# Performance work log

Hardware: AMD Instinct MI355X
Metric: run time of the kernel (lower is better)

## Reference

```python
import jax, jax.numpy as jnp
import numpy as np

BETA = 0.2
ALPHA_NEG = 0.8
ALPHA_POS = 0.2
EPS = 1e-8  # torch cosine_similarity eps

B, D, P = 8192, 256, 4096


def setup_inputs() -> dict:
    key = jax.random.key(0)
    k1, k2 = jax.random.split(key)
    embeddings = jax.random.normal(k1, (B, D), dtype=jnp.float32)
    positive_pairs = jax.random.randint(k2, (P, 2), 0, B, dtype=jnp.int32)
    return {"embeddings": embeddings, "positive_pairs": positive_pairs}


def reference(embeddings, positive_pairs):
    b = embeddings.shape[0]
    p = positive_pairs.shape[0]
    # cosine similarity matrix (normalize once, single GEMM)
    nrm = jnp.maximum(jnp.linalg.norm(embeddings, axis=1, keepdims=True), EPS)
    e = embeddings / nrm
    cos = e @ e.T                              # [B, B]
    exp_cos = jnp.exp(cos / BETA)
    ii = positive_pairs[:, 0]
    jj = positive_pairs[:, 1]
    # mask = eye + positive pairs (both directions)
    mask = jnp.eye(b, dtype=bool)
    mask = mask.at[ii, jj].set(True).at[jj, ii].set(True)
    exp_masked = jnp.where(mask, 0.0, exp_cos)  # masked_fill(mask, 0)
    pos_ij = exp_cos[ii, jj]                   # [P]
    pos_ji = exp_cos[jj, ii]                   # [P]
    exp_i = exp_masked[ii]                     # [P, B]
    exp_j = exp_masked[jj]                     # [P, B]
    # hard-negative mining via alpha_neg quantile per row
    thr_i = jnp.quantile(exp_i, ALPHA_NEG, axis=1, keepdims=True)
    thr_j = jnp.quantile(exp_j, ALPHA_NEG, axis=1, keepdims=True)
    S_i = jnp.sum(jnp.where(exp_i >= thr_i, exp_i, 0.0), axis=1)  # [P]
    S_j = jnp.sum(jnp.where(exp_j >= thr_j, exp_j, 0.0), axis=1)  # [P]
    # hard-positive mining via alpha_pos quantile
    thr_pij = jnp.quantile(pos_ij, ALPHA_POS)
    thr_pji = jnp.quantile(pos_ji, ALPHA_POS)
    sel_ij = pos_ij <= thr_pij
    sel_ji = pos_ji <= thr_pji
    # torch loop zips the two (order-preserving) boolean-selected lists ->
    # truncates to min count; values are never cross-coupled, only the count.
    kmin = jnp.minimum(sel_ij.sum(), sel_ji.sum())
    act_ij = sel_ij & ((jnp.cumsum(sel_ij.astype(jnp.int32)) - 1) < kmin)
    act_ji = sel_ji & ((jnp.cumsum(sel_ji.astype(jnp.int32)) - 1) < kmin)
    # -log(pk / (pk + S[m])) = log1p(S[m] / pk), summed over all m per pk
    term_ij = jnp.log1p(S_i[None, :] / pos_ij[:, None])  # [P, P]
    term_ji = jnp.log1p(S_j[None, :] / pos_ji[:, None])  # [P, P]
    loss = (jnp.sum(term_ij * act_ij[:, None].astype(term_ij.dtype))
            + jnp.sum(term_ji * act_ji[:, None].astype(term_ji.dtype)))
    return loss / (2.0 * p)
```

## Files before the change

### kernel.cpp

```cpp
#include <hip/hip_runtime.h>
#include <stdint.h>

#define BN    8192
#define DK    256
#define PN    4096
#define MAXP  16
#define RANK_ASC 6553
#define QSTEP 0.02f
#define QINV  50.0f

typedef __bf16  bf16_8 __attribute__((ext_vector_type(8)));
typedef __bf16  bf16_4 __attribute__((ext_vector_type(4)));
typedef float   f32x4  __attribute__((ext_vector_type(4)));

__device__ __forceinline__ void gload_lds16(const void* g, void* l) {
  __builtin_amdgcn_global_load_lds(
      (const __attribute__((address_space(1))) unsigned int*)g,
      (__attribute__((address_space(3))) unsigned int*)l, 16, 0, 0);
}

__global__ void prep_clear_kernel(int* pcount, int* rowlist, int* cnt) {
  const int i = blockIdx.x * 256 + threadIdx.x;
  if (i < BN) { pcount[i] = 0; rowlist[i] = 0; }
  if (i == 0) cnt[0] = 0;
}

__global__ void prep_pairs_kernel(const int2* __restrict__ pairs,
                                  int* pcount, int* partners) {
  const int p = blockIdx.x * 256 + threadIdx.x;
  if (p >= PN) return;
  int2 pr = pairs[p];
  int ix = atomicAdd(&pcount[pr.x], 1);
  if (ix < MAXP) partners[pr.x * MAXP + ix] = pr.y;
  int iy = atomicAdd(&pcount[pr.y], 1);
  if (iy < MAXP) partners[pr.y * MAXP + iy] = pr.x;
}

__global__ void prep_compact_kernel(const int* __restrict__ pcount,
                                    int* rowlist, int* cnt) {
  const int i = blockIdx.x * 256 + threadIdx.x;
  if (i < BN && pcount[i] > 0) {
    int pos = atomicAdd(cnt, 1);
    rowlist[pos] = i;
  }
}

__global__ void __launch_bounds__(256) normalize_kernel(
    const float* __restrict__ X, float* __restrict__ E, __bf16* __restrict__ Ebf) {
  const int tid  = threadIdx.x;
  const int lane = tid & 63;
  const int w    = tid >> 6;
  const int row  = blockIdx.x * 4 + w;
  float4 x = ((const float4*)(X + (size_t)row * DK))[lane];
  float ss = x.x * x.x + x.y * x.y + x.z * x.z + x.w * x.w;
  #pragma unroll
  for (int o = 32; o; o >>= 1) ss += __shfl_xor(ss, o);
  float nrm = fmaxf(sqrtf(ss), 1e-8f);
  float4 e;
  e.x = x.x / nrm; e.y = x.y / nrm; e.z = x.z / nrm; e.w = x.w / nrm;
  ((float4*)(E + (size_t)row * DK))[lane] = e;
  bf16_4 b;
  b[0] = (__bf16)e.x; b[1] = (__bf16)e.y; b[2] = (__bf16)e.z; b[3] = (__bf16)e.w;
  *(bf16_4*)(Ebf + (size_t)row * DK + lane * 4) = b;
}

__global__ void __launch_bounds__(256) pos_kernel(
    const float* __restrict__ E, const int2* __restrict__ pairs, float* __restrict__ pos) {
  const int tid  = threadIdx.x;
  const int lane = tid & 63;
  const int w    = tid >> 6;
  const int p    = blockIdx.x * 4 + w;
  int2 pr = pairs[p];
  float4 a = ((const float4*)(E + (size_t)pr.x * DK))[lane];
  float4 b = ((const float4*)(E + (size_t)pr.y * DK))[lane];
  float d = a.x * b.x + a.y * b.y + a.z * b.z + a.w * b.w;
  #pragma unroll
  for (int o = 32; o; o >>= 1) d += __shfl_xor(d, o);
  if (lane == 0) pos[p] = __expf(5.0f * d);
}

__device__ __forceinline__ void find_bin_256(const unsigned* hist, int rank,
                                             int* sh, unsigned* wtot) {
  const int tid = threadIdx.x, lane = tid & 63, w = tid >> 6;
  unsigned x = hist[tid];
  unsigned pref = x;
  #pragma unroll
  for (int o = 1; o < 64; o <<= 1) {
    unsigned y = __shfl_up(pref, o);
    if (lane >= o) pref += y;
  }
  if (lane == 63) wtot[w] = pref;
  __syncthreads();
  unsigned woff = 0;
  for (int i = 0; i < w; ++i) woff += wtot[i];
  unsigned incl = pref + woff, excl = incl - x;
  if ((unsigned)rank >= excl && (unsigned)rank < incl) { sh[0] = tid; sh[1] = rank - (int)excl; }
  __syncthreads();
}

__global__ void __launch_bounds__(256) gemm_code_kernel(
    const __bf16* __restrict__ E, const int* __restrict__ rowlist,
    const int* __restrict__ countp, uint32_t* __restrict__ out4) {
  if ((int)blockIdx.y * 128 >= *countp) return;
  __shared__ __align__(16) __bf16 sA[128 * 32];
  __shared__ __align__(16) __bf16 sB[128 * 32];
  const int tid  = threadIdx.x;
  const int lane = tid & 63;
  const int w    = tid >> 6;
  const int wm   = w >> 1, wn = w & 1;
  const int trow = blockIdx.y * 128;
  const int tcol = blockIdx.x * 128;
  const int r0   = tid >> 2;
  const int seg  = tid & 3;

  const int ga0 = rowlist[trow + r0];
  const int ga1 = rowlist[trow + 64 + r0];
  const __bf16* pa0 = E + (size_t)ga0 * DK + seg * 8;
  const __bf16* pa1 = E + (size_t)ga1 * DK + seg * 8;
  const __bf16* pb0 = E + (size_t)(tcol + r0) * DK + seg * 8;
  const __bf16* pb1 = E + (size_t)(tcol + 64 + r0) * DK + seg * 8;
  __bf16* la0 = &sA[tid * 8];
  __bf16* la1 = &sA[2048 + tid * 8];
  __bf16* lb0 = &sB[tid * 8];
  __bf16* lb1 = &sB[2048 + tid * 8];

  f32x4 acc[4][4];
  #pragma unroll
  for (int i = 0; i < 4; ++i)
    #pragma unroll
    for (int j = 0; j < 4; ++j) {
      f32x4 z = {0.f, 0.f, 0.f, 0.f};
      acc[i][j] = z;
    }

  for (int kt = 0; kt < 8; ++kt) {
    const int k0 = kt * 32;
    __syncthreads();
    gload_lds16(pa0 + k0, la0);
    gload_lds16(pa1 + k0, la1);
    gload_lds16(pb0 + k0, lb0);
    gload_lds16(pb1 + k0, lb1);
    __syncthreads();
    bf16_8 af[4], bfg[4];
    #pragma unroll
    for (int t = 0; t < 4; ++t) {
      af[t]  = *(const bf16_8*)&sA[(wm * 64 + t * 16 + (lane & 15)) * 32 + (lane >> 4) * 8];
      bfg[t] = *(const bf16_8*)&sB[(wn * 64 + t * 16 + (lane & 15)) * 32 + (lane >> 4) * 8];
    }
    #pragma unroll
    for (int i = 0; i < 4; ++i)
      #pragma unroll
      for (int j = 0; j < 4; ++j)
        acc[i][j] = __builtin_amdgcn_mfma_f32_16x16x32_bf16(af[i], bfg[j], acc[i][j], 0, 0, 0);
  }

  const int crow = trow + wm * 64 + (lane >> 4) * 4;
  const int ccol = tcol + wn * 64 + (lane & 15);
  #pragma unroll
  for (int i = 0; i < 4; ++i) {
    const int gidx = (crow + i * 16) >> 2;
    #pragma unroll
    for (int j = 0; j < 4; ++j) {
      const int col = ccol + j * 16;
      uint32_t u = 0;
      #pragma unroll
      for (int r = 0; r < 4; ++r) {
        int c = (int)rintf(fmaf(acc[i][j][r], 250.0f, 128.0f));
        c = c < 1 ? 1 : (c > 255 ? 255 : c);
        u |= (uint32_t)c << (8 * r);
      }
      out4[(size_t)gidx * BN + col] = u;
    }
  }
}

__global__ void __launch_bounds__(256) row_stats4_kernel(
    const uint32_t* __restrict__ expc4, const int* __restrict__ rowlist,
    const int* __restrict__ countp, const int* __restrict__ pcount,
    const int* __restrict__ partners, float* __restrict__ S) {
  __shared__ unsigned hist[4][4][256];
  __shared__ unsigned total[4][256];
  __shared__ int plist[4][MAXP + 1];
  __shared__ int npl[4];
  __shared__ int growl[4];
  __shared__ int sh[2];
  __shared__ unsigned wtot[4];
  __shared__ float redf[4];
  const int g = blockIdx.x;
  const int cnt = *countp;
  if (g * 4 >= cnt) return;
  const int tid = threadIdx.x, lane = tid & 63, w = tid >> 6;

  uint4 rv[8];
  const uint4* src = (const uint4*)(expc4 + (size_t)g * BN);
  #pragma unroll
  for (int q = 0; q < 8; ++q) rv[q] = src[q * 256 + tid];

  if (tid < 4) {
    int rr = g * 4 + tid;
    int grow = (rr < cnt) ? rowlist[rr] : -1;
    growl[tid] = grow;
    int np = 0;
    if (grow >= 0) {
      np = pcount[grow]; if (np > MAXP) np = MAXP;
      for (int e = 0; e < np; ++e) plist[tid][e] = partners[grow * MAXP + e];
      plist[tid][np] = grow;
      np++;
    }
    npl[tid] = np;
  }
  #pragma unroll
  for (int k = 0; k < 16; ++k) ((unsigned*)hist)[k * 256 + tid] = 0;
  __syncthreads();

  #pragma unroll
  for (int r4 = 0; r4 < 4; ++r4) {
    const int np = npl[r4];
    for (int e = 0; e < np; ++e) {
      int c = plist[r4][e];
      int t = c >> 2;
      if ((t & 255) == tid) {
        unsigned* wp = (unsigned*)&rv[t >> 8];
        wp[c & 3] &= ~(0xFFu << (r4 * 8));
      }
    }
  }

  unsigned* h = (unsigned*)hist[w];
  #pragma unroll
  for (int q = 0; q < 8; ++q) {
    #pragma unroll
    for (int word = 0; word < 4; ++word) {
      unsigned dw = ((const unsigned*)&rv[q])[word];
      atomicAdd(&h[0 * 256 + (dw & 255u)], 1u);
      atomicAdd(&h[1 * 256 + ((dw >> 8) & 255u)], 1u);
      atomicAdd(&h[2 * 256 + ((dw >> 16) & 255u)], 1u);
      atomicAdd(&h[3 * 256 + (dw >> 24)], 1u);
    }
  }
  __syncthreads();
  #pragma unroll
  for (int r4 = 0; r4 < 4; ++r4)
    total[r4][tid] = hist[0][r4][tid] + hist[1][r4][tid] + hist[2][r4][tid] + hist[3][r4][tid];
  __syncthreads();

  const float val = __expf((float)(tid - 128) * QSTEP);

  for (int r4 = 0; r4 < 4; ++r4) {
    find_bin_256(total[r4], RANK_ASC, sh, wtot);
    const int b    = sh[0];
    const int need = (int)total[r4][b] - sh[1];
    float contrib = (tid > b) ? (float)total[r4][tid] * val
                  : (tid == b) ? (float)need * val : 0.f;
    #pragma unroll
    for (int o = 32; o; o >>= 1) contrib += __shfl_xor(contrib, o);
    __syncthreads();
    if (lane == 0) redf[w] = contrib;
    __syncthreads();
    if (tid == 0 && growl[r4] >= 0)
      S[growl[r4]] = redf[0] + redf[1] + redf[2] + redf[3];
    __syncthreads();
  }
}

__device__ __forceinline__ float block_sum4(float x, float* red4) {
  const int lane = threadIdx.x & 63, w = threadIdx.x >> 6;
  #pragma unroll
  for (int o = 32; o; o >>= 1) x += __shfl_xor(x, o);
  __syncthreads();
  if (lane == 0) red4[w] = x;
  __syncthreads();
  return red4[0] + red4[1] + red4[2] + red4[3];
}

__global__ void __launch_bounds__(256) finale_kernel(
    const float* __restrict__ pos, const int2* __restrict__ pairs,
    const float* __restrict__ S, float* __restrict__ out) {
  __shared__ uint32_t v[PN];
  __shared__ unsigned hist[256];
  __shared__ int sh[2];
  __shared__ unsigned wtot[4];
  __shared__ float red4[4];
  const int tid = threadIdx.x;
  for (int i = tid; i < PN; i += 256) v[i] = ((const uint32_t*)pos)[i];
  __syncthreads();

  int rank = 819;
  uint32_t prefix = 0;
  for (int pass = 0; pass < 4; ++pass) {
    const int shift = 24 - pass * 8;
    hist[tid] = 0;
    __syncthreads();
    for (int i = tid; i < PN; i += 256) {
      uint32_t x = v[i];
      bool match = (pass == 0) || ((x >> (shift + 8)) == (prefix >> (shift + 8)));
      if (match) atomicAdd(&hist[(x >> shift) & 255u], 1u);
    }
    __syncthreads();
    find_bin_256(hist, rank, sh, wtot);
    prefix |= ((uint32_t)sh[0]) << shift;
    rank = sh[1];
    __syncthreads();
  }
  float thr; __builtin_memcpy(&thr, &prefix, 4);

  float n = 0.f, sl = 0.f, sp = 0.f, sp2 = 0.f;
  for (int r = tid; r < PN; r += 256) {
    float p; uint32_t b = v[r]; __builtin_memcpy(&p, &b, 4);
    if (p <= thr) { n += 1.f; sl += __logf(p); sp += p; sp2 += p * p; }
  }
  float t = 0.f, u = 0.f, vv = 0.f;
  for (int c = tid; c < PN; c += 256) {
    int2 pr = pairs[c];
    float s1 = S[pr.x], s2 = S[pr.y];
    float i1 = 1.f / s1, i2 = 1.f / s2;
    t += __logf(s1) + __logf(s2);
    u += i1 + i2;
    vv += i1 * i1 + i2 * i2;
  }
  const float N  = block_sum4(n, red4);
  const float SL = block_sum4(sl, red4);
  const float SP = block_sum4(sp, red4);
  const float SP2= block_sum4(sp2, red4);
  const float T  = block_sum4(t, red4);
  const float U  = block_sum4(u, red4);
  const float V  = block_sum4(vv, red4);
  if (tid == 0) {
    double num = (double)N * T - 2.0 * (double)PN * (double)SL
               + (double)SP * U - 0.5 * (double)SP2 * V;
    out[0] = (float)(num / (2.0 * (double)PN));
  }
}

extern "C" void kernel_launch(void* const* d_in, const int* in_sizes, int n_in,
                              void* d_out, int out_size, void* d_ws, size_t ws_size,
                              hipStream_t stream) {
  const float* emb  = (const float*)d_in[0];
  const int2* pairs = (const int2*)d_in[1];
  float* out = (float*)d_out;

  char* w = (char*)d_ws;
  size_t off = 0;
  float*    E     = (float*)(w + off);    off += (size_t)BN * DK * 4;
  __bf16*   Ebf   = (__bf16*)(w + off);   off += (size_t)BN * DK * 2;
  float*    S     = (float*)(w + off);    off += (size_t)BN * 4;
  float*    pos   = (float*)(w + off);    off += (size_t)PN * 4;
  int*      pcnt  = (int*)(w + off);      off += (size_t)BN * 4;
  int*      parts = (int*)(w + off);      off += (size_t)BN * MAXP * 4;
  int*      rlist = (int*)(w + off);      off += (size_t)BN * 4;
  int*      cnt   = (int*)(w + off);      off += 256;
  uint32_t* expc4 = (uint32_t*)(w + off); off += (size_t)(BN / 4) * BN * 4;

  prep_clear_kernel<<<BN / 256, 256, 0, stream>>>(pcnt, rlist, cnt);
  normalize_kernel<<<BN / 4, 256, 0, stream>>>(emb, E, Ebf);
  prep_pairs_kernel<<<PN / 256, 256, 0, stream>>>(pairs, pcnt, parts);
  prep_compact_kernel<<<BN / 256, 256, 0, stream>>>(pcnt, rlist, cnt);
  pos_kernel<<<PN / 4, 256, 0, stream>>>(E, pairs, pos);
  gemm_code_kernel<<<dim3(BN / 128, BN / 128), 256, 0, stream>>>(Ebf, rlist, cnt, expc4);
  row_stats4_kernel<<<BN / 4, 256, 0, stream>>>(expc4, rlist, cnt, pcnt, parts, S);
  finale_kernel<<<1, 256, 0, stream>>>(pos, pairs, S, out);
}
```

Baseline: 166.1 us.

## Fuse all stages into one persistent cooperative kernel with grid syncs

Replaces the eight separate kernel launches with a single cooperative persistent kernel that walks through the stages (clear, normalize/pairs, compact/pos, GEMM tiles, row stats, finale) separated by grid.sync, using a shared-memory union across phases. The aim is to remove launch gaps and tail effects between small kernels. It brings grid-wide barrier costs, a grid capped at 512 blocks with grid-stride tile loops (which may cut GEMM occupancy and latency hiding), and a finale run by a single block while the rest of the grid idles. The old multi-kernel path stays as a fallback if the cooperative launch fails.

Result: slower. 362.8 us (+118.4%).

```diff
diff --git a/kernel.cpp b/kernel.cpp
--- a/kernel.cpp
+++ b/kernel.cpp
@@ -1,5 +1,8 @@
 #include <hip/hip_runtime.h>
+#include <hip/hip_cooperative_groups.h>
 #include <stdint.h>
+
+namespace cg = cooperative_groups;
 
 #define BN    8192
 #define DK    256
@@ -7,7 +10,8 @@
 #define MAXP  16
 #define RANK_ASC 6553
 #define QSTEP 0.02f
-#define QINV  50.0f
+#define MAXGRID 512
+#define NCU   256
 
 typedef __bf16  bf16_8 __attribute__((ext_vector_type(8)));
 typedef __bf16  bf16_4 __attribute__((ext_vector_type(4)));
@@ -17,6 +21,308 @@
   __builtin_amdgcn_global_load_lds(
       (const __attribute__((address_space(1))) unsigned int*)g,
       (__attribute__((address_space(3))) unsigned int*)l, 16, 0, 0);
+}
+
+__device__ __forceinline__ void find_bin_256(const unsigned* hist, int rank,
+                                             int* sh, unsigned* wtot) {
+  const int tid = threadIdx.x, lane = tid & 63, w = tid >> 6;
+  unsigned x = hist[tid];
+  unsigned pref = x;
+  #pragma unroll
+  for (int o = 1; o < 64; o <<= 1) {
+    unsigned y = __shfl_up(pref, o);
+    if (lane >= o) pref += y;
+  }
+  if (lane == 63) wtot[w] = pref;
+  __syncthreads();
+  unsigned woff = 0;
+  for (int i = 0; i < w; ++i) woff += wtot[i];
+  unsigned incl = pref + woff, excl = incl - x;
+  if ((unsigned)rank >= excl && (unsigned)rank < incl) { sh[0] = tid; sh[1] = rank - (int)excl; }
+  __syncthreads();
+}
+
+__device__ __forceinline__ float block_sum4(float x, float* red4) {
+  const int lane = threadIdx.x & 63, w = threadIdx.x >> 6;
+  #pragma unroll
+  for (int o = 32; o; o >>= 1) x += __shfl_xor(x, o);
+  __syncthreads();
+  if (lane == 0) red4[w] = x;
+  __syncthreads();
+  return red4[0] + red4[1] + red4[2] + red4[3];
+}
+
+struct Params {
+  const float* emb; const int2* pairs;
+  float* E; __bf16* Ebf; float* S; float* pos;
+  int* pcnt; int* parts; int* rlist; int* cnt;
+  uint32_t* out4; float* out;
+};
+
+union __align__(16) SMem {
+  struct { __bf16 A[128 * 32]; __bf16 B[128 * 32]; } g;
+  struct { unsigned hist[4][4][256]; unsigned total[4][256];
+           int plist[4][MAXP + 1]; int npl[4]; int growl[4];
+           int sh[2]; unsigned wtot[4]; float redf[4]; } rs;
+  struct { uint32_t v[PN]; unsigned hist[256];
+           int sh[2]; unsigned wtot[4]; float red4[4]; } fin;
+};
+
+__global__ void __launch_bounds__(256, 2) mega_kernel(Params prm) {
+  __shared__ SMem sm;
+  cg::grid_group grid = cg::this_grid();
+  const int tid  = threadIdx.x;
+  const int lane = tid & 63;
+  const int wib  = tid >> 6;
+  const int nthr  = gridDim.x * 256;
+  const int nwave = gridDim.x * 4;
+  const int gix  = blockIdx.x * 256 + tid;
+  const int wv   = blockIdx.x * 4 + wib;
+
+  for (int i = gix; i < BN; i += nthr) { prm.pcnt[i] = 0; prm.rlist[i] = 0; }
+  if (gix == 0) prm.cnt[0] = 0;
+  grid.sync();
+
+  for (int row = wv; row < BN; row += nwave) {
+    float4 x = ((const float4*)(prm.emb + (size_t)row * DK))[lane];
+    float ss = x.x * x.x + x.y * x.y + x.z * x.z + x.w * x.w;
+    #pragma unroll
+    for (int o = 32; o; o >>= 1) ss += __shfl_xor(ss, o);
+    float nrm = fmaxf(sqrtf(ss), 1e-8f);
+    float4 e;
+    e.x = x.x / nrm; e.y = x.y / nrm; e.z = x.z / nrm; e.w = x.w / nrm;
+    ((float4*)(prm.E + (size_t)row * DK))[lane] = e;
+    bf16_4 b;
+    b[0] = (__bf16)e.x; b[1] = (__bf16)e.y; b[2] = (__bf16)e.z; b[3] = (__bf16)e.w;
+    *(bf16_4*)(prm.Ebf + (size_t)row * DK + lane * 4) = b;
+  }
+  for (int p = gix; p < PN; p += nthr) {
+    int2 pr = prm.pairs[p];
+    int ix = atomicAdd(&prm.pcnt[pr.x], 1);
+    if (ix < MAXP) prm.parts[pr.x * MAXP + ix] = pr.y;
+    int iy = atomicAdd(&prm.pcnt[pr.y], 1);
+    if (iy < MAXP) prm.parts[pr.y * MAXP + iy] = pr.x;
+  }
+  grid.sync();
+
+  for (int i = gix; i < BN; i += nthr) {
+    if (prm.pcnt[i] > 0) {
+      int pos = atomicAdd(prm.cnt, 1);
+      prm.rlist[pos] = i;
+    }
+  }
+  for (int p = wv; p < PN; p += nwave) {
+    int2 pr = prm.pairs[p];
+    float4 a = ((const float4*)(prm.E + (size_t)pr.x * DK))[lane];
+    float4 b = ((const float4*)(prm.E + (size_t)pr.y * DK))[lane];
+    float d = a.x * b.x + a.y * b.y + a.z * b.z + a.w * b.w;
+    #pragma unroll
+    for (int o = 32; o; o >>= 1) d += __shfl_xor(d, o);
+    if (lane == 0) prm.pos[p] = __expf(5.0f * d);
+  }
+  grid.sync();
+
+  {
+    const int cnt   = prm.cnt[0];
+    const int nrb   = (cnt + 127) >> 7;
+    const int ntile = nrb * (BN / 128);
+    const int wm = wib >> 1, wn = wib & 1;
+    const int r0  = tid >> 2;
+    const int seg = tid & 3;
+    __bf16* la0 = &sm.g.A[tid * 8];
+    __bf16* la1 = &sm.g.A[2048 + tid * 8];
+    __bf16* lb0 = &sm.g.B[tid * 8];
+    __bf16* lb1 = &sm.g.B[2048 + tid * 8];
+
+    for (int t = blockIdx.x; t < ntile; t += gridDim.x) {
+      const int trow = (t >> 6) * 128;
+      const int tcol = (t & 63) * 128;
+      const int ga0 = prm.rlist[trow + r0];
+      const int ga1 = prm.rlist[trow + 64 + r0];
+      const __bf16* pa0 = prm.Ebf + (size_t)ga0 * DK + seg * 8;
+      const __bf16* pa1 = prm.Ebf + (size_t)ga1 * DK + seg * 8;
+      const __bf16* pb0 = prm.Ebf + (size_t)(tcol + r0) * DK + seg * 8;
+      const __bf16* pb1 = prm.Ebf + (size_t)(tcol + 64 + r0) * DK + seg * 8;
+
+      f32x4 acc[4][4];
+      #pragma unroll
+      for (int i = 0; i < 4; ++i)
+        #pragma unroll
+        for (int j = 0; j < 4; ++j) {
+          f32x4 z = {0.f, 0.f, 0.f, 0.f};
+          acc[i][j] = z;
+        }
+
+      for (int kt = 0; kt < 8; ++kt) {
+        const int k0 = kt * 32;
+        __syncthreads();
+        gload_lds16(pa0 + k0, la0);
+        gload_lds16(pa1 + k0, la1);
+        gload_lds16(pb0 + k0, lb0);
+        gload_lds16(pb1 + k0, lb1);
+        __syncthreads();
+        bf16_8 af[4], bfg[4];
+        #pragma unroll
+        for (int q = 0; q < 4; ++q) {
+          af[q]  = *(const bf16_8*)&sm.g.A[(wm * 64 + q * 16 + (lane & 15)) * 32 + (lane >> 4) * 8];
+          bfg[q] = *(const bf16_8*)&sm.g.B[(wn * 64 + q * 16 + (lane & 15)) * 32 + (lane >> 4) * 8];
+        }
+        #pragma unroll
+        for (int i = 0; i < 4; ++i)
+          #pragma unroll
+          for (int j = 0; j < 4; ++j)
+            acc[i][j] = __builtin_amdgcn_mfma_f32_16x16x32_bf16(af[i], bfg[j], acc[i][j], 0, 0, 0);
+      }
+
+      const int crow = trow + wm * 64 + (lane >> 4) * 4;
+      const int ccol = tcol + wn * 64 + (lane & 15);
+      #pragma unroll
+      for (int i = 0; i < 4; ++i) {
+        const int gidx = (crow + i * 16) >> 2;
+        #pragma unroll
+        for (int j = 0; j < 4; ++j) {
+          const int col = ccol + j * 16;
+          uint32_t u = 0;
+          #pragma unroll
+          for (int r = 0; r < 4; ++r) {
+            int c = (int)rintf(fmaf(acc[i][j][r], 250.0f, 128.0f));
+            c = c < 1 ? 1 : (c > 255 ? 255 : c);
+            u |= (uint32_t)c << (8 * r);
+          }
+          prm.out4[(size_t)gidx * BN + col] = u;
+        }
+      }
+    }
+  }
+  grid.sync();
+
+  {
+    const int cnt = prm.cnt[0];
+    for (int g = blockIdx.x; g * 4 < cnt; g += gridDim.x) {
+      __syncthreads();
+      uint4 rv[8];
+      const uint4* src = (const uint4*)(prm.out4 + (size_t)g * BN);
+      #pragma unroll
+      for (int q = 0; q < 8; ++q) rv[q] = src[q * 256 + tid];
+
+      if (tid < 4) {
+        int rr = g * 4 + tid;
+        int grow = (rr < cnt) ? prm.rlist[rr] : -1;
+        sm.rs.growl[tid] = grow;
+        int np = 0;
+        if (grow >= 0) {
+          np = prm.pcnt[grow]; if (np > MAXP) np = MAXP;
+          for (int e = 0; e < np; ++e) sm.rs.plist[tid][e] = prm.parts[grow * MAXP + e];
+          sm.rs.plist[tid][np] = grow;
+          np++;
+        }
+        sm.rs.npl[tid] = np;
+      }
+      #pragma unroll
+      for (int k = 0; k < 16; ++k) ((unsigned*)sm.rs.hist)[k * 256 + tid] = 0;
+      __syncthreads();
+
+      #pragma unroll
+      for (int r4 = 0; r4 < 4; ++r4) {
+        const int np = sm.rs.npl[r4];
+        for (int e = 0; e < np; ++e) {
+          int c = sm.rs.plist[r4][e];
+          int t = c >> 2;
+          if ((t & 255) == tid) {
+            unsigned* wp = (unsigned*)&rv[t >> 8];
+            wp[c & 3] &= ~(0xFFu << (r4 * 8));
+          }
+        }
+      }
+
+      unsigned* h = (unsigned*)sm.rs.hist[wib];
+      #pragma unroll
+      for (int q = 0; q < 8; ++q) {
+        #pragma unroll
+        for (int word = 0; word < 4; ++word) {
+          unsigned dw = ((const unsigned*)&rv[q])[word];
+          atomicAdd(&h[0 * 256 + (dw & 255u)], 1u);
+          atomicAdd(&h[1 * 256 + ((dw >> 8) & 255u)], 1u);
+          atomicAdd(&h[2 * 256 + ((dw >> 16) & 255u)], 1u);
+          atomicAdd(&h[3 * 256 + (dw >> 24)], 1u);
+        }
+      }
+      __syncthreads();
+      #pragma unroll
+      for (int r4 = 0; r4 < 4; ++r4)
+        sm.rs.total[r4][tid] = sm.rs.hist[0][r4][tid] + sm.rs.hist[1][r4][tid]
+                             + sm.rs.hist[2][r4][tid] + sm.rs.hist[3][r4][tid];
+      __syncthreads();
+
+      const float val = __expf((float)(tid - 128) * QSTEP);
+      for (int r4 = 0; r4 < 4; ++r4) {
+        find_bin_256(sm.rs.total[r4], RANK_ASC, sm.rs.sh, sm.rs.wtot);
+        const int b    = sm.rs.sh[0];
+        const int need = (int)sm.rs.total[r4][b] - sm.rs.sh[1];
+        float contrib = (tid > b) ? (float)sm.rs.total[r4][tid] * val
+                      : (tid == b) ? (float)need * val : 0.f;
+        #pragma unroll
+        for (int o = 32; o; o >>= 1) contrib += __shfl_xor(contrib, o);
+        __syncthreads();
+        if (lane == 0) sm.rs.redf[wib] = contrib;
+        __syncthreads();
+        if (tid == 0 && sm.rs.growl[r4] >= 0)
+          prm.S[sm.rs.growl[r4]] = sm.rs.redf[0] + sm.rs.redf[1] + sm.rs.redf[2] + sm.rs.redf[3];
+        __syncthreads();
+      }
+    }
+  }
+  grid.sync();
+
+  if (blockIdx.x == 0) {
+    for (int i = tid; i < PN; i += 256) sm.fin.v[i] = ((const uint32_t*)prm.pos)[i];
+    __syncthreads();
+    int rank = 819;
+    uint32_t prefix = 0;
+    for (int pass = 0; pass < 4; ++pass) {
+      const int shift = 24 - pass * 8;
+      sm.fin.hist[tid] = 0;
+      __syncthreads();
+      for (int i = tid; i < PN; i += 256) {
+        uint32_t x = sm.fin.v[i];
+        bool match = (pass == 0) || ((x >> (shift + 8)) == (prefix >> (shift + 8)));
+        if (match) atomicAdd(&sm.fin.hist[(x >> shift) & 255u], 1u);
+      }
+      __syncthreads();
+      find_bin_256(sm.fin.hist, rank, sm.fin.sh, sm.fin.wtot);
+      prefix |= ((uint32_t)sm.fin.sh[0]) << shift;
+      rank = sm.fin.sh[1];
+      __syncthreads();
+    }
+    float thr; __builtin_memcpy(&thr, &prefix, 4);
+
+    float n = 0.f, sl = 0.f, sp = 0.f, sp2 = 0.f;
+    for (int r = tid; r < PN; r += 256) {
+      float p; uint32_t b = sm.fin.v[r]; __builtin_memcpy(&p, &b, 4);
+      if (p <= thr) { n += 1.f; sl += __logf(p); sp += p; sp2 += p * p; }
+    }
+    float t = 0.f, u = 0.f, vv = 0.f;
+    for (int c = tid; c < PN; c += 256) {
+      int2 pr = prm.pairs[c];
+      float s1 = prm.S[pr.x], s2 = prm.S[pr.y];
+      float i1 = 1.f / s1, i2 = 1.f / s2;
+      t += __logf(s1) + __logf(s2);
+      u += i1 + i2;
+      vv += i1 * i1 + i2 * i2;
+    }
+    const float N   = block_sum4(n, sm.fin.red4);
+    const float SL  = block_sum4(sl, sm.fin.red4);
+    const float SP  = block_sum4(sp, sm.fin.red4);
+    const float SP2 = block_sum4(sp2, sm.fin.red4);
+    const float T   = block_sum4(t, sm.fin.red4);
+    const float U   = block_sum4(u, sm.fin.red4);
+    const float V   = block_sum4(vv, sm.fin.red4);
+    if (tid == 0) {
+      double num = (double)N * T - 2.0 * (double)PN * (double)SL
+                 + (double)SP * U - 0.5 * (double)SP2 * V;
+      prm.out[0] = (float)(num / (2.0 * (double)PN));
+    }
+  }
 }
 
 __global__ void prep_clear_kernel(int* pcount, int* rowlist, int* cnt) {
@@ -77,25 +383,6 @@
   #pragma unroll
   for (int o = 32; o; o >>= 1) d += __shfl_xor(d, o);
   if (lane == 0) pos[p] = __expf(5.0f * d);
-}
-
-__device__ __forceinline__ void find_bin_256(const unsigned* hist, int rank,
-                                             int* sh, unsigned* wtot) {
-  const int tid = threadIdx.x, lane = tid & 63, w = tid >> 6;
-  unsigned x = hist[tid];
-  unsigned pref = x;
-  #pragma unroll
-  for (int o = 1; o < 64; o <<= 1) {
-    unsigned y = __shfl_up(pref, o);
-    if (lane >= o) pref += y;
-  }
-  if (lane == 63) wtot[w] = pref;
-  __syncthreads();
-  unsigned woff = 0;
-  for (int i = 0; i < w; ++i) woff += wtot[i];
-  unsigned incl = pref + woff, excl = incl - x;
-  if ((unsigned)rank >= excl && (unsigned)rank < incl) { sh[0] = tid; sh[1] = rank - (int)excl; }
-  __syncthreads();
 }
 
 __global__ void __launch_bounds__(256) gemm_code_kernel(
@@ -143,9 +430,9 @@
     __syncthreads();
     bf16_8 af[4], bfg[4];
     #pragma unroll
-    for (int t = 0; t < 4; ++t) {
-      af[t]  = *(const bf16_8*)&sA[(wm * 64 + t * 16 + (lane & 15)) * 32 + (lane >> 4) * 8];
-      bfg[t] = *(const bf16_8*)&sB[(wn * 64 + t * 16 + (lane & 15)) * 32 + (lane >> 4) * 8];
+    for (int q = 0; q < 4; ++q) {
+      af[q]  = *(const bf16_8*)&sA[(wm * 64 + q * 16 + (lane & 15)) * 32 + (lane >> 4) * 8];
+      bfg[q] = *(const bf16_8*)&sB[(wn * 64 + q * 16 + (lane & 15)) * 32 + (lane >> 4) * 8];
     }
     #pragma unroll
     for (int i = 0; i < 4; ++i)
@@ -245,7 +532,6 @@
   __syncthreads();
 
   const float val = __expf((float)(tid - 128) * QSTEP);
-
   for (int r4 = 0; r4 < 4; ++r4) {
     find_bin_256(total[r4], RANK_ASC, sh, wtot);
     const int b    = sh[0];
@@ -261,16 +547,6 @@
       S[growl[r4]] = redf[0] + redf[1] + redf[2] + redf[3];
     __syncthreads();
   }
-}
-
-__device__ __forceinline__ float block_sum4(float x, float* red4) {
-  const int lane = threadIdx.x & 63, w = threadIdx.x >> 6;
-  #pragma unroll
-  for (int o = 32; o; o >>= 1) x += __shfl_xor(x, o);
-  __syncthreads();
-  if (lane == 0) red4[w] = x;
-  __syncthreads();
-  return red4[0] + red4[1] + red4[2] + red4[3];
 }
 
 __global__ void __launch_bounds__(256) finale_kernel(
@@ -284,7 +560,6 @@
   const int tid = threadIdx.x;
   for (int i = tid; i < PN; i += 256) v[i] = ((const uint32_t*)pos)[i];
   __syncthreads();
-
   int rank = 819;
   uint32_t prefix = 0;
   for (int pass = 0; pass < 4; ++pass) {
@@ -318,13 +593,13 @@
     u += i1 + i2;
     vv += i1 * i1 + i2 * i2;
   }
-  const float N  = block_sum4(n, red4);
-  const float SL = block_sum4(sl, red4);
-  const float SP = block_sum4(sp, red4);
-  const float SP2= block_sum4(sp2, red4);
-  const float T  = block_sum4(t, red4);
-  const float U  = block_sum4(u, red4);
-  const float V  = block_sum4(vv, red4);
+  const float N   = block_sum4(n, red4);
+  const float SL  = block_sum4(sl, red4);
+  const float SP  = block_sum4(sp, red4);
+  const float SP2 = block_sum4(sp2, red4);
+  const float T   = block_sum4(t, red4);
+  const float U   = block_sum4(u, red4);
+  const float V   = block_sum4(vv, red4);
   if (tid == 0) {
     double num = (double)N * T - 2.0 * (double)PN * (double)SL
                + (double)SP * U - 0.5 * (double)SP2 * V;
@@ -335,10 +610,6 @@
 extern "C" void kernel_launch(void* const* d_in, const int* in_sizes, int n_in,
                               void* d_out, int out_size, void* d_ws, size_t ws_size,
                               hipStream_t stream) {
-  const float* emb  = (const float*)d_in[0];
-  const int2* pairs = (const int2*)d_in[1];
-  float* out = (float*)d_out;
-
   char* w = (char*)d_ws;
   size_t off = 0;
   float*    E     = (float*)(w + off);    off += (size_t)BN * DK * 4;
@@ -349,14 +620,32 @@
   int*      parts = (int*)(w + off);      off += (size_t)BN * MAXP * 4;
   int*      rlist = (int*)(w + off);      off += (size_t)BN * 4;
   int*      cnt   = (int*)(w + off);      off += 256;
-  uint32_t* expc4 = (uint32_t*)(w + off); off += (size_t)(BN / 4) * BN * 4;
-
-  prep_clear_kernel<<<BN / 256, 256, 0, stream>>>(pcnt, rlist, cnt);
-  normalize_kernel<<<BN / 4, 256, 0, stream>>>(emb, E, Ebf);
-  prep_pairs_kernel<<<PN / 256, 256, 0, stream>>>(pairs, pcnt, parts);
-  prep_compact_kernel<<<BN / 256, 256, 0, stream>>>(pcnt, rlist, cnt);
-  pos_kernel<<<PN / 4, 256, 0, stream>>>(E, pairs, pos);
-  gemm_code_kernel<<<dim3(BN / 128, BN / 128), 256, 0, stream>>>(Ebf, rlist, cnt, expc4);
-  row_stats4_kernel<<<BN / 4, 256, 0, stream>>>(expc4, rlist, cnt, pcnt, parts, S);
-  finale_kernel<<<1, 256, 0, stream>>>(pos, pairs, S, out);
-}
+  uint32_t* out4  = (uint32_t*)(w + off); off += (size_t)(BN / 4) * BN * 4;
+
+  Params prm;
+  prm.emb   = (const float*)d_in[0];
+  prm.pairs = (const int2*)d_in[1];
+  prm.E = E; prm.Ebf = Ebf; prm.S = S; prm.pos = pos;
+  prm.pcnt = pcnt; prm.parts = parts; prm.rlist = rlist; prm.cnt = cnt;
+  prm.out4 = out4; prm.out = (float*)d_out;
+
+  int maxB = 0;
+  hipError_t qerr = hipOccupancyMaxActiveBlocksPerMultiprocessor(&maxB, mega_kernel, 256, 0);
+  int grid = (qerr == hipSuccess && maxB > 0) ? maxB * NCU : NCU;
+  if (grid > MAXGRID) grid = MAXGRID;
+
+  void* kargs[] = { &prm };
+  hipError_t lerr = hipLaunchCooperativeKernel((const void*)mega_kernel,
+                                               dim3(grid), dim3(256), kargs, 0, stream);
+  if (lerr != hipSuccess) {
+    (void)hipGetLastError();
+    prep_clear_kernel<<<BN / 256, 256, 0, stream>>>(pcnt, rlist, cnt);
+    normalize_kernel<<<BN / 4, 256, 0, stream>>>((const float*)d_in[0], E, Ebf);
+    prep_pairs_kernel<<<PN / 256, 256, 0, stream>>>((const int2*)d_in[1], pcnt, parts);
+    prep_compact_kernel<<<BN / 256, 256, 0, stream>>>(pcnt, rlist, cnt);
+    pos_kernel<<<PN / 4, 256, 0, stream>>>(E, (const int2*)d_in[1], pos);
+    gemm_code_kernel<<<dim3(BN / 128, BN / 128), 256, 0, stream>>>(Ebf, rlist, cnt, out4);
+    row_stats4_kernel<<<BN / 4, 256, 0, stream>>>(out4, rlist, cnt, pcnt, parts, S);
+    finale_kernel<<<1, 256, 0, stream>>>(pos, (const int2*)d_in[1], S, (float*)d_out);
+  }
+}
```
